# Kernel tuning notes

Hardware: AMD Instinct MI355X
Metric: run time of the kernel (lower is better)

## Reference

```python
import jax, jax.numpy as jnp
import numpy as np

MARGIN = 5.0  # margin_between_clusters


def setup_inputs() -> dict:
    key = jax.random.key(0)
    k1, k2, k3 = jax.random.split(key, 3)
    N, D, K = 262144, 128, 64
    embeddings = jax.random.normal(k1, (N, D), dtype=jnp.float32)
    cluster_labels = jax.random.randint(k2, (N,), 0, K, dtype=jnp.int64)
    centroids = jax.random.normal(k3, (K, D), dtype=jnp.float32)
    return {"embeddings": embeddings, "cluster_labels": cluster_labels, "centroids": centroids}


def reference(embeddings, cluster_labels, centroids):
    # Assumes all K clusters are present in cluster_labels (true w.h.p. for N >> K),
    # matching number_cluster = len(unique(labels)) in the original.
    N, d = embeddings.shape
    K = centroids.shape[0]
    labels = cluster_labels.astype(jnp.int32)

    x2 = jnp.sum(embeddings * embeddings, axis=1, keepdims=True)        # [N,1]
    c2 = jnp.sum(centroids * centroids, axis=1)[None, :]                # [1,K]
    d2 = jnp.maximum(x2 + c2 - 2.0 * (embeddings @ centroids.T), 0.0)  # [N,K]
    dist = jnp.sqrt(d2)

    rows = jnp.arange(N)
    own_d = dist[rows, labels]                 # distance to own centroid
    counts = jax.ops.segment_sum(jnp.ones((N,), embeddings.dtype), labels, num_segments=K)
    safe_counts = jnp.maximum(counts, 1.0)

    # attraction: per cluster, mean of squared distance to own centroid
    attr_per_cluster = jax.ops.segment_sum(own_d * own_d, labels, num_segments=K) / safe_counts
    attraction_loss = jnp.sum(jnp.where(counts > 0, attr_per_cluster, 0.0))

    # repulsion: per cluster, mean over (points_in_cluster x other_centroids) of relu((m - d)^2)
    rep = jax.nn.relu((MARGIN - dist) ** 2)    # [N,K]
    row_other = (jnp.sum(rep, axis=1) - rep[rows, labels]) / (K - 1)
    rep_per_cluster = jax.ops.segment_sum(row_other, labels, num_segments=K) / safe_counts
    repulsion_loss = jnp.sum(jnp.where(counts > 0, rep_per_cluster, 0.0))

    return (attraction_loss + repulsion_loss) / K
```

## Files before the change

### kernel.cpp

```cpp
#include <hip/hip_runtime.h>


constexpr int N = 262144;
constexpr int D = 128;
constexpr int K = 64;

constexpr int GRID = 2048;
constexpr int PANEL = 34 * 32;

typedef __bf16 bf16x4 __attribute__((ext_vector_type(4)));
typedef __bf16 bf16x8 __attribute__((ext_vector_type(8)));
typedef float  f32x16 __attribute__((ext_vector_type(16)));

__global__ __launch_bounds__(256) void dcl_main(
    const float* __restrict__ emb,
    const int*   __restrict__ labels,
    const float* __restrict__ cent,
    float* __restrict__ g_attr,
    float* __restrict__ g_rep,
    int*   __restrict__ g_cnt)
{
    __shared__ bf16x8 sA[2 * 8 * 64];
    __shared__ __align__(16) bf16x4 sPanel[4 * PANEL];
    __shared__ float  s_c2[K];
    __shared__ __align__(16) float sC2i0[2][16];
    __shared__ __align__(16) float sC2i1[2][16];
    __shared__ float  s_attr[K];
    __shared__ float  s_rep[K];
    __shared__ int    s_cnt[K];

    const int tid  = threadIdx.x;
    const int wave = tid >> 6;
    const int lane = tid & 63;
    const int l31  = lane & 31;
    const int h    = lane >> 5;

    const int tile = blockIdx.x * 4 + wave;

    float4 buf[16];
    {
        const float4* src = (const float4*)emb + (size_t)tile * 1024 + lane;
        #pragma unroll
        for (int q = 0; q < 16; ++q) buf[q] = src[q * 64];
    }
    const int lbl = labels[tile * 32 + l31];

    #pragma unroll
    for (int e = tid; e < 2 * 8 * 64; e += 256) {
        const int t = e >> 9, s = (e >> 6) & 7, l = e & 63;
        const int c  = t * 32 + (l & 31);
        const int d0 = 16 * s + 8 * (l >> 5);
        const float4 f0 = *(const float4*)(cent + c * D + d0);
        const float4 f1 = *(const float4*)(cent + c * D + d0 + 4);
        bf16x8 v;
        v[0] = (__bf16)f0.x; v[1] = (__bf16)f0.y; v[2] = (__bf16)f0.z; v[3] = (__bf16)f0.w;
        v[4] = (__bf16)f1.x; v[5] = (__bf16)f1.y; v[6] = (__bf16)f1.z; v[7] = (__bf16)f1.w;
        sA[e] = v;
    }
    if (tid < K) {
        const float4* cp = (const float4*)(cent + tid * D);
        float sa = 0.f, sb = 0.f;
        #pragma unroll
        for (int q = 0; q < D / 8; ++q) {
            const float4 f = cp[2 * q];
            const float4 g = cp[2 * q + 1];
            sa = fmaf(f.x, f.x, sa); sa = fmaf(f.y, f.y, sa);
            sa = fmaf(f.z, f.z, sa); sa = fmaf(f.w, f.w, sa);
            sb = fmaf(g.x, g.x, sb); sb = fmaf(g.y, g.y, sb);
            sb = fmaf(g.z, g.z, sb); sb = fmaf(g.w, g.w, sb);
        }
        s_c2[tid] = sa + sb;
        s_attr[tid] = 0.f; s_rep[tid] = 0.f; s_cnt[tid] = 0;
    }
    __syncthreads();
    if (tid < 32) {
        const int hh = tid >> 4, r = tid & 15;
        const int rb = (r & 3) + 8 * (r >> 2) + 4 * hh;
        sC2i0[hh][r] = -0.5f * s_c2[rb];
        sC2i1[hh][r] = -0.5f * s_c2[rb + 32];
    }
    __syncthreads();

    bf16x4* panel = sPanel + wave * PANEL;

    #pragma unroll
    for (int q = 0; q < 16; ++q) {
        bf16x4 v;
        v[0] = (__bf16)buf[q].x; v[1] = (__bf16)buf[q].y;
        v[2] = (__bf16)buf[q].z; v[3] = (__bf16)buf[q].w;
        const int n = 2 * q + h;
        panel[34 * n + l31] = v;
    }

    f32x16 acc0, acc1;
    {
        const float4* p0 = (const float4*)&sC2i0[h][0];
        const float4* p1 = (const float4*)&sC2i1[h][0];
        #pragma unroll
        for (int w = 0; w < 4; ++w) {
            ((float4*)&acc0)[w] = p0[w];
            ((float4*)&acc1)[w] = p1[w];
        }
    }

    float x2A = 0.f, x2B = 0.f;
    #pragma unroll
    for (int s = 0; s < 8; ++s) {
        const bf16x8 b = *(const bf16x8*)&panel[34 * l31 + 4 * s + 2 * h];
        {
            const float e0 = (float)b[0], e1 = (float)b[1], e2 = (float)b[2], e3 = (float)b[3];
            const float e4 = (float)b[4], e5 = (float)b[5], e6 = (float)b[6], e7 = (float)b[7];
            float p0 = e0 * e0; p0 = fmaf(e1, e1, p0); p0 = fmaf(e2, e2, p0); p0 = fmaf(e3, e3, p0);
            float p1 = e4 * e4; p1 = fmaf(e5, e5, p1); p1 = fmaf(e6, e6, p1); p1 = fmaf(e7, e7, p1);
            x2A += p0; x2B += p1;
        }
        const bf16x8 a0 = sA[s * 64 + lane];
        const bf16x8 a1 = sA[(8 + s) * 64 + lane];
        acc0 = __builtin_amdgcn_mfma_f32_32x32x16_bf16(a0, b, acc0, 0, 0, 0);
        acc1 = __builtin_amdgcn_mfma_f32_32x32x16_bf16(a1, b, acc1, 0, 0, 0);
    }

    const float x2p = x2A + x2B;
    const float x2 = x2p + __shfl_xor(x2p, 32);

    float s1a = 0.f, s1b = 0.f, s2a = 0.f, s2b = 0.f, own = 0.f;
    #pragma unroll
    for (int r = 0; r < 16; ++r) {
        const int rbase = (r & 3) + 8 * (r >> 2) + 4 * h;
        {
            float d2 = fmaf(-2.f, acc0[r], x2);
            d2 = fmaxf(d2, 0.f);
            const float dd = __builtin_amdgcn_sqrtf(d2);
            s1a += dd; s2a += d2;
            if (rbase == lbl) own += d2;
        }
        {
            float d2 = fmaf(-2.f, acc1[r], x2);
            d2 = fmaxf(d2, 0.f);
            const float dd = __builtin_amdgcn_sqrtf(d2);
            s1b += dd; s2b += d2;
            if (rbase + 32 == lbl) own += d2;
        }
    }
    float s1 = s1a + s1b, s2 = s2a + s2b;
    s1  += __shfl_xor(s1, 32);
    s2  += __shfl_xor(s2, 32);
    own += __shfl_xor(own, 32);

    if (lane < 32) {
        const float down = __builtin_amdgcn_sqrtf(own);
        const float own_term = fmaf(-10.f, down, 25.f) + own;
        const float row_other = (25.f * K - 10.f * s1 + s2 - own_term) * (1.f / (K - 1));
        atomicAdd(&s_attr[lbl], own);
        atomicAdd(&s_rep[lbl], row_other);
        atomicAdd(&s_cnt[lbl], 1);
    }

    __syncthreads();
    if (tid < K) {
        const int rep8 = (blockIdx.x & 7) * K;
        atomicAdd(&g_attr[rep8 + tid], s_attr[tid]);
        atomicAdd(&g_rep[rep8 + tid], s_rep[tid]);
        atomicAdd(&g_cnt[rep8 + tid], s_cnt[tid]);
    }
}

__global__ void dcl_finish(const float* __restrict__ g_attr,
                           const float* __restrict__ g_rep,
                           const int*   __restrict__ g_cnt,
                           float* __restrict__ out)
{
    const int k = threadIdx.x;
    float a = 0.f, r = 0.f;
    int   c = 0;
    #pragma unroll
    for (int j = 0; j < 8; ++j) {
        a += g_attr[j * K + k];
        r += g_rep[j * K + k];
        c += g_cnt[j * K + k];
    }
    float v = (c > 0) ? (a + r) / (float)c : 0.f;
    #pragma unroll
    for (int off = 32; off > 0; off >>= 1) v += __shfl_down(v, off);
    if (k == 0) out[0] = v * (1.f / K);
}

extern "C" void kernel_launch(void* const* d_in, const int* in_sizes, int n_in,
                              void* d_out, int out_size, void* d_ws, size_t ws_size,
                              hipStream_t stream) {
    const float* emb    = (const float*)d_in[0];
    const int*   labels = (const int*)d_in[1];
    const float* cent   = (const float*)d_in[2];
    float* out = (float*)d_out;

    float* g_attr = (float*)d_ws;
    float* g_rep  = g_attr + 8 * K;
    int*   g_cnt  = (int*)(g_rep + 8 * K);

    hipMemsetAsync(d_ws, 0, 3 * 8 * K * sizeof(float), stream);
    dcl_main<<<GRID, 256, 0, stream>>>(emb, labels, cent, g_attr, g_rep, g_cnt);
    dcl_finish<<<1, 64, 0, stream>>>(g_attr, g_rep, g_cnt, out);
}
```

Before: 209.9 us.

## Process four tiles per wave with double-buffered register prefetch

Each wave now handles four 32-row tiles instead of one, and the grid shrinks from 2048 to 512 blocks. The next tile's embeddings are loaded into a second register buffer while the current tile's MFMA work and reduction run. This spreads the per-block setup (centroid bf16 conversion, c2 norms, block-level atomics) over more rows and hides global load latency. The cost is doubled register buffers, with launch bounds set to 2 blocks per SM, which may limit occupancy or cause spills, and fewer blocks in flight to cover memory latency.

```diff
diff --git a/kernel.cpp b/kernel.cpp
--- a/kernel.cpp
+++ b/kernel.cpp
@@ -5,14 +5,15 @@
 constexpr int D = 128;
 constexpr int K = 64;
 
-constexpr int GRID = 2048;
+constexpr int GRID = 512;
+constexpr int TPW  = 4;
 constexpr int PANEL = 34 * 32;
 
 typedef __bf16 bf16x4 __attribute__((ext_vector_type(4)));
 typedef __bf16 bf16x8 __attribute__((ext_vector_type(8)));
 typedef float  f32x16 __attribute__((ext_vector_type(16)));
 
-__global__ __launch_bounds__(256) void dcl_main(
+__global__ __launch_bounds__(256, 2) void dcl_main(
     const float* __restrict__ emb,
     const int*   __restrict__ labels,
     const float* __restrict__ cent,
@@ -35,15 +36,18 @@
     const int l31  = lane & 31;
     const int h    = lane >> 5;
 
-    const int tile = blockIdx.x * 4 + wave;
-
-    float4 buf[16];
+    const int g     = blockIdx.x * 4 + wave;
+    const int base  = g * TPW;
+
+    float4 bufA[16], bufB[16];
     {
-        const float4* src = (const float4*)emb + (size_t)tile * 1024 + lane;
-        #pragma unroll
-        for (int q = 0; q < 16; ++q) buf[q] = src[q * 64];
-    }
-    const int lbl = labels[tile * 32 + l31];
+        const float4* src = (const float4*)emb + (size_t)base * 1024 + lane;
+        #pragma unroll
+        for (int q = 0; q < 16; ++q) bufA[q] = src[q * 64];
+    }
+    int lbl[TPW];
+    #pragma unroll
+    for (int t = 0; t < TPW; ++t) lbl[t] = labels[(base + t) * 32 + l31];
 
     #pragma unroll
     for (int e = tid; e < 2 * 8 * 64; e += 256) {
@@ -63,11 +67,11 @@
         #pragma unroll
         for (int q = 0; q < D / 8; ++q) {
             const float4 f = cp[2 * q];
-            const float4 g = cp[2 * q + 1];
+            const float4 gg = cp[2 * q + 1];
             sa = fmaf(f.x, f.x, sa); sa = fmaf(f.y, f.y, sa);
             sa = fmaf(f.z, f.z, sa); sa = fmaf(f.w, f.w, sa);
-            sb = fmaf(g.x, g.x, sb); sb = fmaf(g.y, g.y, sb);
-            sb = fmaf(g.z, g.z, sb); sb = fmaf(g.w, g.w, sb);
+            sb = fmaf(gg.x, gg.x, sb); sb = fmaf(gg.y, gg.y, sb);
+            sb = fmaf(gg.z, gg.z, sb); sb = fmaf(gg.w, gg.w, sb);
         }
         s_c2[tid] = sa + sb;
         s_attr[tid] = 0.f; s_rep[tid] = 0.f; s_cnt[tid] = 0;
@@ -84,76 +88,90 @@
     bf16x4* panel = sPanel + wave * PANEL;
 
     #pragma unroll
-    for (int q = 0; q < 16; ++q) {
-        bf16x4 v;
-        v[0] = (__bf16)buf[q].x; v[1] = (__bf16)buf[q].y;
-        v[2] = (__bf16)buf[q].z; v[3] = (__bf16)buf[q].w;
-        const int n = 2 * q + h;
-        panel[34 * n + l31] = v;
-    }
-
-    f32x16 acc0, acc1;
-    {
-        const float4* p0 = (const float4*)&sC2i0[h][0];
-        const float4* p1 = (const float4*)&sC2i1[h][0];
-        #pragma unroll
-        for (int w = 0; w < 4; ++w) {
-            ((float4*)&acc0)[w] = p0[w];
-            ((float4*)&acc1)[w] = p1[w];
-        }
-    }
-
-    float x2A = 0.f, x2B = 0.f;
-    #pragma unroll
-    for (int s = 0; s < 8; ++s) {
-        const bf16x8 b = *(const bf16x8*)&panel[34 * l31 + 4 * s + 2 * h];
+    for (int t = 0; t < TPW; ++t) {
+        float4* cur = (t & 1) ? bufB : bufA;
+        float4* nxt = (t & 1) ? bufA : bufB;
+
+        #pragma unroll
+        for (int q = 0; q < 16; ++q) {
+            bf16x4 v;
+            v[0] = (__bf16)cur[q].x; v[1] = (__bf16)cur[q].y;
+            v[2] = (__bf16)cur[q].z; v[3] = (__bf16)cur[q].w;
+            const int n = 2 * q + h;
+            panel[34 * n + l31] = v;
+        }
+
+        if (t + 1 < TPW) {
+            const float4* src = (const float4*)emb + (size_t)(base + t + 1) * 1024 + lane;
+            #pragma unroll
+            for (int q = 0; q < 16; ++q) nxt[q] = src[q * 64];
+        }
+        __builtin_amdgcn_sched_barrier(0);
+
+        f32x16 acc0, acc1;
         {
-            const float e0 = (float)b[0], e1 = (float)b[1], e2 = (float)b[2], e3 = (float)b[3];
-            const float e4 = (float)b[4], e5 = (float)b[5], e6 = (float)b[6], e7 = (float)b[7];
-            float p0 = e0 * e0; p0 = fmaf(e1, e1, p0); p0 = fmaf(e2, e2, p0); p0 = fmaf(e3, e3, p0);
-            float p1 = e4 * e4; p1 = fmaf(e5, e5, p1); p1 = fmaf(e6, e6, p1); p1 = fmaf(e7, e7, p1);
-            x2A += p0; x2B += p1;
-        }
-        const bf16x8 a0 = sA[s * 64 + lane];
-        const bf16x8 a1 = sA[(8 + s) * 64 + lane];
-        acc0 = __builtin_amdgcn_mfma_f32_32x32x16_bf16(a0, b, acc0, 0, 0, 0);
-        acc1 = __builtin_amdgcn_mfma_f32_32x32x16_bf16(a1, b, acc1, 0, 0, 0);
-    }
-
-    const float x2p = x2A + x2B;
-    const float x2 = x2p + __shfl_xor(x2p, 32);
-
-    float s1a = 0.f, s1b = 0.f, s2a = 0.f, s2b = 0.f, own = 0.f;
-    #pragma unroll
-    for (int r = 0; r < 16; ++r) {
-        const int rbase = (r & 3) + 8 * (r >> 2) + 4 * h;
-        {
-            float d2 = fmaf(-2.f, acc0[r], x2);
-            d2 = fmaxf(d2, 0.f);
-            const float dd = __builtin_amdgcn_sqrtf(d2);
-            s1a += dd; s2a += d2;
-            if (rbase == lbl) own += d2;
-        }
-        {
-            float d2 = fmaf(-2.f, acc1[r], x2);
-            d2 = fmaxf(d2, 0.f);
-            const float dd = __builtin_amdgcn_sqrtf(d2);
-            s1b += dd; s2b += d2;
-            if (rbase + 32 == lbl) own += d2;
-        }
-    }
-    float s1 = s1a + s1b, s2 = s2a + s2b;
-    s1  += __shfl_xor(s1, 32);
-    s2  += __shfl_xor(s2, 32);
-    own += __shfl_xor(own, 32);
-
-    if (lane < 32) {
-        const float down = __builtin_amdgcn_sqrtf(own);
-        const float own_term = fmaf(-10.f, down, 25.f) + own;
-        const float row_other = (25.f * K - 10.f * s1 + s2 - own_term) * (1.f / (K - 1));
-        atomicAdd(&s_attr[lbl], own);
-        atomicAdd(&s_rep[lbl], row_other);
-        atomicAdd(&s_cnt[lbl], 1);
+            const float4* p0 = (const float4*)&sC2i0[h][0];
+            const float4* p1 = (const float4*)&sC2i1[h][0];
+            #pragma unroll
+            for (int w = 0; w < 4; ++w) {
+                ((float4*)&acc0)[w] = p0[w];
+                ((float4*)&acc1)[w] = p1[w];
+            }
+        }
+
+        float x2A = 0.f, x2B = 0.f;
+        #pragma unroll
+        for (int s = 0; s < 8; ++s) {
+            const bf16x8 b = *(const bf16x8*)&panel[34 * l31 + 4 * s + 2 * h];
+            {
+                const float e0 = (float)b[0], e1 = (float)b[1], e2 = (float)b[2], e3 = (float)b[3];
+                const float e4 = (float)b[4], e5 = (float)b[5], e6 = (float)b[6], e7 = (float)b[7];
+                float p0 = e0 * e0; p0 = fmaf(e1, e1, p0); p0 = fmaf(e2, e2, p0); p0 = fmaf(e3, e3, p0);
+                float p1 = e4 * e4; p1 = fmaf(e5, e5, p1); p1 = fmaf(e6, e6, p1); p1 = fmaf(e7, e7, p1);
+                x2A += p0; x2B += p1;
+            }
+            const bf16x8 a0 = sA[s * 64 + lane];
+            const bf16x8 a1 = sA[(8 + s) * 64 + lane];
+            acc0 = __builtin_amdgcn_mfma_f32_32x32x16_bf16(a0, b, acc0, 0, 0, 0);
+            acc1 = __builtin_amdgcn_mfma_f32_32x32x16_bf16(a1, b, acc1, 0, 0, 0);
+        }
+
+        const float x2p = x2A + x2B;
+        const float x2 = x2p + __shfl_xor(x2p, 32);
+        const int li = lbl[t];
+
+        float s1a = 0.f, s1b = 0.f, s2a = 0.f, s2b = 0.f, own = 0.f;
+        #pragma unroll
+        for (int r = 0; r < 16; ++r) {
+            const int rbase = (r & 3) + 8 * (r >> 2) + 4 * h;
+            {
+                float d2 = fmaf(-2.f, acc0[r], x2);
+                d2 = fmaxf(d2, 0.f);
+                const float dd = __builtin_amdgcn_sqrtf(d2);
+                s1a += dd; s2a += d2;
+                if (rbase == li) own += d2;
+            }
+            {
+                float d2 = fmaf(-2.f, acc1[r], x2);
+                d2 = fmaxf(d2, 0.f);
+                const float dd = __builtin_amdgcn_sqrtf(d2);
+                s1b += dd; s2b += d2;
+                if (rbase + 32 == li) own += d2;
+            }
+        }
+        float s1 = s1a + s1b, s2 = s2a + s2b;
+        s1  += __shfl_xor(s1, 32);
+        s2  += __shfl_xor(s2, 32);
+        own += __shfl_xor(own, 32);
+
+        if (lane < 32) {
+            const float down = __builtin_amdgcn_sqrtf(own);
+            const float own_term = fmaf(-10.f, down, 25.f) + own;
+            const float row_other = (25.f * K - 10.f * s1 + s2 - own_term) * (1.f / (K - 1));
+            atomicAdd(&s_attr[li], own);
+            atomicAdd(&s_rep[li], row_other);
+            atomicAdd(&s_cnt[li], 1);
+        }
     }
 
     __syncthreads();
```

New measurement: 199.3 us. -5.1%, faster.
